# Kernel optimization log

Hardware: AMD Instinct MI355X
Metric: run time of the kernel (lower is better)

Reference implementation:

```python
import jax, jax.numpy as jnp
import numpy as np

N_NODES = 100000
N_EDGES = 3200000
NFEAT = 256
NHID = 256


def setup_inputs() -> dict:
    key = jax.random.key(0)
    ks = jax.random.split(key, 8)
    x = jax.random.normal(ks[0], (N_NODES, NFEAT), dtype=jnp.float32)
    # Glorot-ish scaled weights
    W1 = jax.random.normal(ks[1], (NFEAT, NHID), dtype=jnp.float32) / np.sqrt(NFEAT)
    b1 = jax.random.normal(ks[2], (NHID,), dtype=jnp.float32) * 0.01
    W2 = jax.random.normal(ks[3], (NHID, NHID), dtype=jnp.float32) / np.sqrt(NHID)
    b2 = jax.random.normal(ks[4], (NHID,), dtype=jnp.float32) * 0.01
    edge_weight = jax.random.uniform(ks[5], (N_EDGES,), dtype=jnp.float32)
    edge_src = jax.random.randint(ks[6], (N_EDGES,), 0, N_NODES, dtype=jnp.int32)
    edge_dst = jax.random.randint(ks[7], (N_EDGES,), 0, N_NODES, dtype=jnp.int32)
    return {
        "x": x, "W1": W1, "b1": b1, "W2": W2, "b2": b2,
        "edge_weight": edge_weight, "edge_src": edge_src, "edge_dst": edge_dst,
    }


def _gcn_layer(x, W, b, edge_weight, edge_src, edge_dst):
    # support = x @ W  (dense GEMM, [N, d_out])
    support = x @ W
    # spmm(adj, support): gather source rows, scale by edge weight, scatter-add to dst
    msgs = support[edge_src] * edge_weight[:, None]          # [E, d_out]
    agg = jax.ops.segment_sum(msgs, edge_dst, num_segments=N_NODES)
    return agg + b


def reference(x, W1, b1, W2, b2, edge_weight, edge_src, edge_dst):
    # Eval mode: F.dropout is identity (training=False).
    h = jax.nn.elu(_gcn_layer(x, W1, b1, edge_weight, edge_src, edge_dst))
    h = jax.nn.elu(_gcn_layer(h, W2, b2, edge_weight, edge_src, edge_dst))
    return h
```

## Files before the change

### kernel.cpp

```cpp
#include <hip/hip_runtime.h>
#include <math.h>

#define N_NODES 100000
#define N_EDGES 3200000
#define NF 256

typedef unsigned short u16;
typedef unsigned int u32;

typedef __bf16 bf16x8_t __attribute__((ext_vector_type(8)));
typedef float f32x4_t __attribute__((ext_vector_type(4)));

__device__ __forceinline__ float bf2f(u16 u) {
  union { u32 i; float f; } v; v.i = ((u32)u) << 16; return v.f;
}
__device__ __forceinline__ u16 f2bf(float f) {
  union { float f; u32 i; } v; v.f = f;
  u32 x = v.i;
  u32 r = (x + 0x7FFFu + ((x >> 16) & 1u)) >> 16;
  return (u16)r;
}

__global__ void sniff_kernel(const u16* __restrict__ xr, int* __restrict__ flag) {
  __shared__ int cnt;
  if (threadIdx.x == 0) cnt = 0;
  __syncthreads();
  int c = 0;
  for (int i = threadIdx.x; i < 65536; i += 256) {
    u16 u = xr[i];
    if ((u & 0x7F80u) == 0x7F80u) c++;
  }
  atomicAdd(&cnt, c);
  __syncthreads();
  if (threadIdx.x == 0) flag[0] = (cnt >= 4) ? 1 : 0;
}

__global__ void transpose_w(const u16* __restrict__ Wu, const float* __restrict__ Wf,
                            const int* __restrict__ flagp, u16* __restrict__ Wt) {
  int k = blockIdx.x;
  int n = threadIdx.x;
  if (flagp[0]) Wt[n * NF + k] = f2bf(Wf[k * NF + n]);
  else          Wt[n * NF + k] = Wu[k * NF + n];
}

__global__ void conv_bias(const u16* __restrict__ bu, const float* __restrict__ bf_,
                          const int* __restrict__ flagp, u16* __restrict__ o) {
  int i = threadIdx.x;
  if (flagp[0]) o[i] = f2bf(bf_[i]);
  else          o[i] = bu[i];
}

__global__ void copy_i32(const int* __restrict__ a, int* __restrict__ b, int n) {
  int i = blockIdx.x * 256 + threadIdx.x;
  if (i < n) b[i] = a[i];
}

__global__ void hist_kernel(const int* __restrict__ dst, int* __restrict__ counts) {
  int e = blockIdx.x * 256 + threadIdx.x;
  atomicAdd(&counts[dst[e]], 1);
}

__global__ void scanA(const int* __restrict__ counts, int* __restrict__ partial) {
  __shared__ int s[256];
  int t = threadIdx.x;
  int gid = blockIdx.x * 256 + t;
  int v = (gid < N_NODES) ? counts[gid] : 0;
  s[t] = v;
  __syncthreads();
  for (int offd = 128; offd > 0; offd >>= 1) {
    if (t < offd) s[t] += s[t + offd];
    __syncthreads();
  }
  if (t == 0) partial[blockIdx.x] = s[0];
}

__global__ void scanB(int* __restrict__ partial) {
  const int NPART = 391;
  __shared__ int s[512];
  int t = threadIdx.x;
  int v = (t < NPART) ? partial[t] : 0;
  s[t] = v;
  __syncthreads();
  for (int offd = 1; offd < 512; offd <<= 1) {
    int x = 0;
    if (t >= offd) x = s[t - offd];
    __syncthreads();
    s[t] += x;
    __syncthreads();
  }
  if (t < NPART) partial[t] = (t == 0) ? 0 : s[t - 1];
}

__global__ void scanC(const int* __restrict__ counts, const int* __restrict__ partial,
                      int* __restrict__ offs) {
  __shared__ int s[256];
  int t = threadIdx.x;
  int b = blockIdx.x;
  int gid = b * 256 + t;
  int v = (gid < N_NODES) ? counts[gid] : 0;
  s[t] = v;
  __syncthreads();
  for (int offd = 1; offd < 256; offd <<= 1) {
    int x = 0;
    if (t >= offd) x = s[t - offd];
    __syncthreads();
    s[t] += x;
    __syncthreads();
  }
  int incl = s[t];
  if (gid < N_NODES) offs[gid] = partial[b] + (incl - v);
  if (gid == N_NODES - 1) offs[N_NODES] = partial[b] + incl;
}

__global__ void scatter_full(const int* __restrict__ src, const int* __restrict__ dst,
                             const u16* __restrict__ wu, const float* __restrict__ wf,
                             const int* __restrict__ flagp, int* __restrict__ cursor,
                             int* __restrict__ ssrc, u16* __restrict__ sw) {
  int e = blockIdx.x * 256 + threadIdx.x;
  int d = dst[e];
  int pos = atomicAdd(&cursor[d], 1);
  ssrc[pos] = src[e];
  if (flagp[0]) sw[pos] = f2bf(wf[e]);
  else          sw[pos] = wu[e];
}

__global__ void scatter_eid(const int* __restrict__ dst, int* __restrict__ cursor,
                            int* __restrict__ seid) {
  int e = blockIdx.x * 256 + threadIdx.x;
  int d = dst[e];
  int pos = atomicAdd(&cursor[d], 1);
  seid[pos] = e;
}

__global__ __launch_bounds__(256) void gemm_bf16(
    const u16* __restrict__ A2, const float* __restrict__ A4,
    const u16* __restrict__ Bt, u16* __restrict__ C, int M,
    const int* __restrict__ flagp, int amask) {
  __shared__ __align__(16) u16 Al[128][40];
  __shared__ __align__(16) u16 Bl[128][40];
  const int afl = amask ? flagp[0] : 0;
  const int tid = threadIdx.x;
  const int m0 = blockIdx.x * 128;
  const int n0 = blockIdx.y * 128;
  const int lane = tid & 63;
  const int wave = tid >> 6;
  const int wm = (wave & 1) * 64;
  const int wn = (wave >> 1) * 64;
  const int mrow = lane & 15;
  const int grp = lane >> 4;

  f32x4_t acc[4][4];
  const f32x4_t zero = {0.f, 0.f, 0.f, 0.f};
#pragma unroll
  for (int i = 0; i < 4; ++i)
#pragma unroll
    for (int j = 0; j < 4; ++j) acc[i][j] = zero;

  for (int k0 = 0; k0 < NF; k0 += 32) {
#pragma unroll
    for (int r = 0; r < 2; ++r) {
      int chunk = tid + 256 * r;
      int row = chunk >> 2;
      int col = (chunk & 3) * 8;
      int gm = m0 + row;
      if (afl) {
        u16 t8[8];
        if (gm < M) {
          const float* p = A4 + (size_t)gm * NF + k0 + col;
          float4 ua = *(const float4*)(p);
          float4 ub = *(const float4*)(p + 4);
          t8[0] = f2bf(ua.x); t8[1] = f2bf(ua.y); t8[2] = f2bf(ua.z); t8[3] = f2bf(ua.w);
          t8[4] = f2bf(ub.x); t8[5] = f2bf(ub.y); t8[6] = f2bf(ub.z); t8[7] = f2bf(ub.w);
        } else {
          for (int q = 0; q < 8; ++q) t8[q] = 0;
        }
        *(uint4*)(&Al[row][col]) = *(const uint4*)t8;
      } else {
        uint4 va = make_uint4(0u, 0u, 0u, 0u);
        if (gm < M) va = *(const uint4*)(A2 + (size_t)gm * NF + k0 + col);
        *(uint4*)(&Al[row][col]) = va;
      }
      uint4 vb = *(const uint4*)(Bt + (size_t)(n0 + row) * NF + k0 + col);
      *(uint4*)(&Bl[row][col]) = vb;
    }
    __syncthreads();
    bf16x8_t af[4], bfr[4];
#pragma unroll
    for (int i = 0; i < 4; ++i)
      af[i] = *(const bf16x8_t*)(&Al[wm + i * 16 + mrow][grp * 8]);
#pragma unroll
    for (int j = 0; j < 4; ++j)
      bfr[j] = *(const bf16x8_t*)(&Bl[wn + j * 16 + mrow][grp * 8]);
#pragma unroll
    for (int i = 0; i < 4; ++i)
#pragma unroll
      for (int j = 0; j < 4; ++j)
        acc[i][j] = __builtin_amdgcn_mfma_f32_16x16x32_bf16(af[i], bfr[j], acc[i][j], 0, 0, 0);
    __syncthreads();
  }

#pragma unroll
  for (int i = 0; i < 4; ++i) {
#pragma unroll
    for (int j = 0; j < 4; ++j) {
#pragma unroll
      for (int r = 0; r < 4; ++r) {
        int row = m0 + wm + i * 16 + grp * 4 + r;
        int col = n0 + wn + j * 16 + mrow;
        if (row < M) C[(size_t)row * NF + col] = f2bf(acc[i][j][r]);
      }
    }
  }
}

__global__ __launch_bounds__(256) void agg_full(
    const u16* __restrict__ sup, const int* __restrict__ offs,
    const int* __restrict__ ssrc, const u16* __restrict__ sw,
    const u16* __restrict__ bbf, u16* __restrict__ out2, float* __restrict__ out4,
    const int* __restrict__ flagp, int outmask) {
  int node = blockIdx.x * 4 + (threadIdx.x >> 6);
  int lane = threadIdx.x & 63;
  int c0 = lane * 4;
  float a0 = 0.f, a1 = 0.f, a2 = 0.f, a3 = 0.f;
  int e = offs[node];
  int eend = offs[node + 1];

  for (; e + 8 <= eend; e += 8) {
    int s0 = ssrc[e + 0], s1 = ssrc[e + 1], s2 = ssrc[e + 2], s3 = ssrc[e + 3];
    int s4 = ssrc[e + 4], s5 = ssrc[e + 5], s6 = ssrc[e + 6], s7 = ssrc[e + 7];
    float w0 = bf2f(sw[e + 0]), w1 = bf2f(sw[e + 1]), w2 = bf2f(sw[e + 2]), w3 = bf2f(sw[e + 3]);
    float w4 = bf2f(sw[e + 4]), w5 = bf2f(sw[e + 5]), w6 = bf2f(sw[e + 6]), w7 = bf2f(sw[e + 7]);
    ushort4 v0 = *(const ushort4*)(sup + (size_t)s0 * NF + c0);
    ushort4 v1 = *(const ushort4*)(sup + (size_t)s1 * NF + c0);
    ushort4 v2 = *(const ushort4*)(sup + (size_t)s2 * NF + c0);
    ushort4 v3 = *(const ushort4*)(sup + (size_t)s3 * NF + c0);
    ushort4 v4 = *(const ushort4*)(sup + (size_t)s4 * NF + c0);
    ushort4 v5 = *(const ushort4*)(sup + (size_t)s5 * NF + c0);
    ushort4 v6 = *(const ushort4*)(sup + (size_t)s6 * NF + c0);
    ushort4 v7 = *(const ushort4*)(sup + (size_t)s7 * NF + c0);
    a0 += bf2f(v0.x) * w0; a1 += bf2f(v0.y) * w0; a2 += bf2f(v0.z) * w0; a3 += bf2f(v0.w) * w0;
    a0 += bf2f(v1.x) * w1; a1 += bf2f(v1.y) * w1; a2 += bf2f(v1.z) * w1; a3 += bf2f(v1.w) * w1;
    a0 += bf2f(v2.x) * w2; a1 += bf2f(v2.y) * w2; a2 += bf2f(v2.z) * w2; a3 += bf2f(v2.w) * w2;
    a0 += bf2f(v3.x) * w3; a1 += bf2f(v3.y) * w3; a2 += bf2f(v3.z) * w3; a3 += bf2f(v3.w) * w3;
    a0 += bf2f(v4.x) * w4; a1 += bf2f(v4.y) * w4; a2 += bf2f(v4.z) * w4; a3 += bf2f(v4.w) * w4;
    a0 += bf2f(v5.x) * w5; a1 += bf2f(v5.y) * w5; a2 += bf2f(v5.z) * w5; a3 += bf2f(v5.w) * w5;
    a0 += bf2f(v6.x) * w6; a1 += bf2f(v6.y) * w6; a2 += bf2f(v6.z) * w6; a3 += bf2f(v6.w) * w6;
    a0 += bf2f(v7.x) * w7; a1 += bf2f(v7.y) * w7; a2 += bf2f(v7.z) * w7; a3 += bf2f(v7.w) * w7;
  }
  for (; e < eend; ++e) {
    int src = ssrc[e];
    float w = bf2f(sw[e]);
    ushort4 v = *(const ushort4*)(sup + (size_t)src * NF + c0);
    a0 += bf2f(v.x) * w;
    a1 += bf2f(v.y) * w;
    a2 += bf2f(v.z) * w;
    a3 += bf2f(v.w) * w;
  }
  ushort4 bv = *(const ushort4*)(bbf + c0);
  float r0 = a0 + bf2f(bv.x);
  float r1 = a1 + bf2f(bv.y);
  float r2 = a2 + bf2f(bv.z);
  float r3 = a3 + bf2f(bv.w);
  r0 = r0 > 0.f ? r0 : expm1f(r0);
  r1 = r1 > 0.f ? r1 : expm1f(r1);
  r2 = r2 > 0.f ? r2 : expm1f(r2);
  r3 = r3 > 0.f ? r3 : expm1f(r3);
  if (outmask && flagp[0]) {
    float4 o4;
    o4.x = r0; o4.y = r1; o4.z = r2; o4.w = r3;
    *(float4*)(out4 + (size_t)node * NF + c0) = o4;
  } else {
    ushort4 o;
    o.x = f2bf(r0); o.y = f2bf(r1); o.z = f2bf(r2); o.w = f2bf(r3);
    *(ushort4*)(out2 + (size_t)node * NF + c0) = o;
  }
}

__global__ __launch_bounds__(256) void agg_eid(
    const u16* __restrict__ sup, const int* __restrict__ offs,
    const int* __restrict__ seid, const int* __restrict__ esrc,
    const u16* __restrict__ ewu, const float* __restrict__ ewf,
    const u16* __restrict__ bbf, u16* __restrict__ out2, float* __restrict__ out4,
    const int* __restrict__ flagp, int outmask) {
  int node = blockIdx.x * 4 + (threadIdx.x >> 6);
  int lane = threadIdx.x & 63;
  int c0 = lane * 4;
  int isf = flagp[0];
  float a0 = 0.f, a1 = 0.f, a2 = 0.f, a3 = 0.f;
  int e = offs[node];
  int eend = offs[node + 1];
  for (; e < eend; ++e) {
    int eid = seid[e];
    int src = esrc[eid];
    float w = isf ? ewf[eid] : bf2f(ewu[eid]);
    ushort4 v = *(const ushort4*)(sup + (size_t)src * NF + c0);
    a0 += bf2f(v.x) * w;
    a1 += bf2f(v.y) * w;
    a2 += bf2f(v.z) * w;
    a3 += bf2f(v.w) * w;
  }
  ushort4 bv = *(const ushort4*)(bbf + c0);
  float r0 = a0 + bf2f(bv.x);
  float r1 = a1 + bf2f(bv.y);
  float r2 = a2 + bf2f(bv.z);
  float r3 = a3 + bf2f(bv.w);
  r0 = r0 > 0.f ? r0 : expm1f(r0);
  r1 = r1 > 0.f ? r1 : expm1f(r1);
  r2 = r2 > 0.f ? r2 : expm1f(r2);
  r3 = r3 > 0.f ? r3 : expm1f(r3);
  if (outmask && isf) {
    float4 o4;
    o4.x = r0; o4.y = r1; o4.z = r2; o4.w = r3;
    *(float4*)(out4 + (size_t)node * NF + c0) = o4;
  } else {
    ushort4 o;
    o.x = f2bf(r0); o.y = f2bf(r1); o.z = f2bf(r2); o.w = f2bf(r3);
    *(ushort4*)(out2 + (size_t)node * NF + c0) = o;
  }
}

extern "C" void kernel_launch(void* const* d_in, const int* in_sizes, int n_in,
                              void* d_out, int out_size, void* d_ws, size_t ws_size,
                              hipStream_t stream) {
  const u16* x2    = (const u16*)d_in[0];
  const float* x4  = (const float*)d_in[0];
  const u16* W1u   = (const u16*)d_in[1];
  const float* W1f = (const float*)d_in[1];
  const u16* b1u   = (const u16*)d_in[2];
  const float* b1f = (const float*)d_in[2];
  const u16* W2u   = (const u16*)d_in[3];
  const float* W2f = (const float*)d_in[3];
  const u16* b2u   = (const u16*)d_in[4];
  const float* b2f = (const float*)d_in[4];
  const u16* ewu   = (const u16*)d_in[5];
  const float* ewf = (const float*)d_in[5];
  const int* esrc  = (const int*)d_in[6];
  const int* edst  = (const int*)d_in[7];
  u16* out2  = (u16*)d_out;
  float* out4 = (float*)d_out;

  char* ws = (char*)d_ws;
  size_t oWt1     = 0;
  size_t oWt2     = 131072;
  size_t oSup     = 262144;
  size_t oCounts  = 51462144;
  size_t oOffs    = 51862528;
  size_t oCursor  = 52262912;
  size_t oPartial = 52663296;
  size_t oFlag    = 52665344;
  size_t oBb1     = 52665600;
  size_t oBb2     = 52666624;
  size_t oTail    = 52667648;
  size_t need_full = oTail + 12800000 + 6400000;

  u16* Wt1     = (u16*)(ws + oWt1);
  u16* Wt2     = (u16*)(ws + oWt2);
  u16* sup     = (u16*)(ws + oSup);
  int* counts  = (int*)(ws + oCounts);
  int* offs    = (int*)(ws + oOffs);
  int* cursor  = (int*)(ws + oCursor);
  int* partial = (int*)(ws + oPartial);
  int* flag    = (int*)(ws + oFlag);
  u16* bb1     = (u16*)(ws + oBb1);
  u16* bb2     = (u16*)(ws + oBb2);

  u16* h1 = out2;

  sniff_kernel<<<1, 256, 0, stream>>>(x2, flag);
  hipMemsetAsync(counts, 0, (size_t)N_NODES * 4, stream);
  transpose_w<<<256, 256, 0, stream>>>(W1u, W1f, flag, Wt1);
  transpose_w<<<256, 256, 0, stream>>>(W2u, W2f, flag, Wt2);
  conv_bias<<<1, 256, 0, stream>>>(b1u, b1f, flag, bb1);
  conv_bias<<<1, 256, 0, stream>>>(b2u, b2f, flag, bb2);
  hist_kernel<<<N_EDGES / 256, 256, 0, stream>>>(edst, counts);
  scanA<<<391, 256, 0, stream>>>(counts, partial);
  scanB<<<1, 512, 0, stream>>>(partial);
  scanC<<<391, 256, 0, stream>>>(counts, partial, offs);
  copy_i32<<<391, 256, 0, stream>>>(offs, cursor, N_NODES);

  dim3 ggrid((N_NODES + 127) / 128, 2);

  if (ws_size >= need_full) {
    int* ssrc = (int*)(ws + oTail);
    u16* sw   = (u16*)(ws + oTail + 12800000);
    scatter_full<<<N_EDGES / 256, 256, 0, stream>>>(esrc, edst, ewu, ewf, flag, cursor, ssrc, sw);
    gemm_bf16<<<ggrid, 256, 0, stream>>>(x2, x4, Wt1, sup, N_NODES, flag, 1);
    agg_full<<<N_NODES / 4, 256, 0, stream>>>(sup, offs, ssrc, sw, bb1, h1, out4, flag, 0);
    gemm_bf16<<<ggrid, 256, 0, stream>>>(h1, (const float*)h1, Wt2, sup, N_NODES, flag, 0);
    agg_full<<<N_NODES / 4, 256, 0, stream>>>(sup, offs, ssrc, sw, bb2, out2, out4, flag, 1);
  } else {
    int* seid = (int*)(ws + oTail);
    scatter_eid<<<N_EDGES / 256, 256, 0, stream>>>(edst, cursor, seid);
    gemm_bf16<<<ggrid, 256, 0, stream>>>(x2, x4, Wt1, sup, N_NODES, flag, 1);
    agg_eid<<<N_NODES / 4, 256, 0, stream>>>(sup, offs, seid, esrc, ewu, ewf, bb1, h1, out4, flag, 0);
    gemm_bf16<<<ggrid, 256, 0, stream>>>(h1, (const float*)h1, Wt2, sup, N_NODES, flag, 0);
    agg_eid<<<N_NODES / 4, 256, 0, stream>>>(sup, offs, seid, esrc, ewu, ewf, bb2, out2, out4, flag, 1);
  }
}
```

Baseline: 1.129 ms.

## Use direct-to-LDS loads in GEMM, rank-based CSR build, wider aggregation gathers

Several changes land at once. The histogram pass now records each edge's rank, so the CSR placement becomes atomic-free and the cursor copy is dropped. Fp32 x is pre-converted to bf16 in a separate pass into a scratch region of the output. The GEMM stages tiles with global_load_lds into unpadded LDS, swaps the MFMA operands and stores packed 4-element results. Aggregation has each half-wave handle alternate edges with 16-byte gathers, then combines the halves with a shuffle. The costs are an extra conversion pass, possible LDS bank conflicts from the unpadded layout, and reliance on output-buffer scratch space.

```diff
diff --git a/kernel.cpp b/kernel.cpp
--- a/kernel.cpp
+++ b/kernel.cpp
@@ -10,6 +10,11 @@
 
 typedef __bf16 bf16x8_t __attribute__((ext_vector_type(8)));
 typedef float f32x4_t __attribute__((ext_vector_type(4)));
+
+union U8 { uint4 q; u16 s[8]; };
+
+typedef __attribute__((address_space(1))) const void* as1_cvp;
+typedef __attribute__((address_space(3))) void* as3_vp;
 
 __device__ __forceinline__ float bf2f(u16 u) {
   union { u32 i; float f; } v; v.i = ((u32)u) << 16; return v.f;
@@ -19,6 +24,10 @@
   u32 x = v.i;
   u32 r = (x + 0x7FFFu + ((x >> 16) & 1u)) >> 16;
   return (u16)r;
+}
+
+__device__ __forceinline__ void gload_lds16(const u16* g, u16* l) {
+  __builtin_amdgcn_global_load_lds((as1_cvp)g, (as3_vp)l, 16, 0, 0);
 }
 
 __global__ void sniff_kernel(const u16* __restrict__ xr, int* __restrict__ flag) {
@@ -50,14 +59,22 @@
   else          o[i] = bu[i];
 }
 
-__global__ void copy_i32(const int* __restrict__ a, int* __restrict__ b, int n) {
-  int i = blockIdx.x * 256 + threadIdx.x;
-  if (i < n) b[i] = a[i];
-}
-
-__global__ void hist_kernel(const int* __restrict__ dst, int* __restrict__ counts) {
+__global__ void conv_x(const float* __restrict__ xf, const int* __restrict__ flagp,
+                       u16* __restrict__ xbf) {
+  if (!flagp[0]) return;
+  size_t i = ((size_t)blockIdx.x * 256 + threadIdx.x) * 8;
+  float4 a = *(const float4*)(xf + i);
+  float4 b = *(const float4*)(xf + i + 4);
+  U8 t;
+  t.s[0] = f2bf(a.x); t.s[1] = f2bf(a.y); t.s[2] = f2bf(a.z); t.s[3] = f2bf(a.w);
+  t.s[4] = f2bf(b.x); t.s[5] = f2bf(b.y); t.s[6] = f2bf(b.z); t.s[7] = f2bf(b.w);
+  *(uint4*)(xbf + i) = t.q;
+}
+
+__global__ void hist_rank(const int* __restrict__ dst, int* __restrict__ counts,
+                          int* __restrict__ rank) {
   int e = blockIdx.x * 256 + threadIdx.x;
-  atomicAdd(&counts[dst[e]], 1);
+  rank[e] = atomicAdd(&counts[dst[e]], 1);
 }
 
 __global__ void scanA(const int* __restrict__ counts, int* __restrict__ partial) {
@@ -112,33 +129,31 @@
   if (gid == N_NODES - 1) offs[N_NODES] = partial[b] + incl;
 }
 
-__global__ void scatter_full(const int* __restrict__ src, const int* __restrict__ dst,
-                             const u16* __restrict__ wu, const float* __restrict__ wf,
-                             const int* __restrict__ flagp, int* __restrict__ cursor,
-                             int* __restrict__ ssrc, u16* __restrict__ sw) {
+__global__ void place_full(const int* __restrict__ src, const int* __restrict__ dst,
+                           const u16* __restrict__ wu, const float* __restrict__ wf,
+                           const int* __restrict__ flagp, const int* __restrict__ offs,
+                           const int* __restrict__ rank,
+                           int* __restrict__ ssrc, u16* __restrict__ sw) {
   int e = blockIdx.x * 256 + threadIdx.x;
-  int d = dst[e];
-  int pos = atomicAdd(&cursor[d], 1);
+  int pos = offs[dst[e]] + rank[e];
   ssrc[pos] = src[e];
   if (flagp[0]) sw[pos] = f2bf(wf[e]);
   else          sw[pos] = wu[e];
 }
 
-__global__ void scatter_eid(const int* __restrict__ dst, int* __restrict__ cursor,
-                            int* __restrict__ seid) {
+__global__ void place_eid(const int* __restrict__ dst, const int* __restrict__ offs,
+                          const int* __restrict__ rank, int* __restrict__ seid) {
   int e = blockIdx.x * 256 + threadIdx.x;
-  int d = dst[e];
-  int pos = atomicAdd(&cursor[d], 1);
-  seid[pos] = e;
-}
-
-__global__ __launch_bounds__(256) void gemm_bf16(
-    const u16* __restrict__ A2, const float* __restrict__ A4,
+  seid[offs[dst[e]] + rank[e]] = e;
+}
+
+__global__ __launch_bounds__(256) void gemm_gll(
+    const u16* __restrict__ A0, const u16* __restrict__ A1,
     const u16* __restrict__ Bt, u16* __restrict__ C, int M,
-    const int* __restrict__ flagp, int amask) {
-  __shared__ __align__(16) u16 Al[128][40];
-  __shared__ __align__(16) u16 Bl[128][40];
-  const int afl = amask ? flagp[0] : 0;
+    const int* __restrict__ flagp) {
+  __shared__ __align__(16) u16 Al[128 * 32];
+  __shared__ __align__(16) u16 Bl[128 * 32];
+  const u16* A = flagp[0] ? A1 : A0;
   const int tid = threadIdx.x;
   const int m0 = blockIdx.x * 128;
   const int n0 = blockIdx.y * 128;
@@ -156,59 +171,47 @@
 #pragma unroll
     for (int j = 0; j < 4; ++j) acc[i][j] = zero;
 
+  const int rA = lane >> 2;
+  const int cA = (lane & 3) * 8;
+
   for (int k0 = 0; k0 < NF; k0 += 32) {
 #pragma unroll
-    for (int r = 0; r < 2; ++r) {
-      int chunk = tid + 256 * r;
-      int row = chunk >> 2;
-      int col = (chunk & 3) * 8;
-      int gm = m0 + row;
-      if (afl) {
-        u16 t8[8];
-        if (gm < M) {
-          const float* p = A4 + (size_t)gm * NF + k0 + col;
-          float4 ua = *(const float4*)(p);
-          float4 ub = *(const float4*)(p + 4);
-          t8[0] = f2bf(ua.x); t8[1] = f2bf(ua.y); t8[2] = f2bf(ua.z); t8[3] = f2bf(ua.w);
-          t8[4] = f2bf(ub.x); t8[5] = f2bf(ub.y); t8[6] = f2bf(ub.z); t8[7] = f2bf(ub.w);
-        } else {
-          for (int q = 0; q < 8; ++q) t8[q] = 0;
-        }
-        *(uint4*)(&Al[row][col]) = *(const uint4*)t8;
-      } else {
-        uint4 va = make_uint4(0u, 0u, 0u, 0u);
-        if (gm < M) va = *(const uint4*)(A2 + (size_t)gm * NF + k0 + col);
-        *(uint4*)(&Al[row][col]) = va;
-      }
-      uint4 vb = *(const uint4*)(Bt + (size_t)(n0 + row) * NF + k0 + col);
-      *(uint4*)(&Bl[row][col]) = vb;
+    for (int c = 0; c < 2; ++c) {
+      int r0 = wave * 32 + c * 16;
+      int ar = r0 + rA;
+      int gm = m0 + ar;
+      if (gm >= M) gm = 0;
+      gload_lds16(A + (size_t)gm * NF + k0 + cA, &Al[r0 * 32]);
+      gload_lds16(Bt + (size_t)(n0 + ar) * NF + k0 + cA, &Bl[r0 * 32]);
     }
     __syncthreads();
     bf16x8_t af[4], bfr[4];
 #pragma unroll
     for (int i = 0; i < 4; ++i)
-      af[i] = *(const bf16x8_t*)(&Al[wm + i * 16 + mrow][grp * 8]);
+      af[i] = *(const bf16x8_t*)(&Al[(wm + i * 16 + mrow) * 32 + grp * 8]);
 #pragma unroll
     for (int j = 0; j < 4; ++j)
-      bfr[j] = *(const bf16x8_t*)(&Bl[wn + j * 16 + mrow][grp * 8]);
+      bfr[j] = *(const bf16x8_t*)(&Bl[(wn + j * 16 + mrow) * 32 + grp * 8]);
 #pragma unroll
     for (int i = 0; i < 4; ++i)
 #pragma unroll
       for (int j = 0; j < 4; ++j)
-        acc[i][j] = __builtin_amdgcn_mfma_f32_16x16x32_bf16(af[i], bfr[j], acc[i][j], 0, 0, 0);
+        acc[i][j] = __builtin_amdgcn_mfma_f32_16x16x32_bf16(bfr[j], af[i], acc[i][j], 0, 0, 0);
     __syncthreads();
   }
 
 #pragma unroll
   for (int i = 0; i < 4; ++i) {
+    int row = m0 + wm + i * 16 + mrow;
+    if (row >= M) continue;
 #pragma unroll
     for (int j = 0; j < 4; ++j) {
-#pragma unroll
-      for (int r = 0; r < 4; ++r) {
-        int row = m0 + wm + i * 16 + grp * 4 + r;
-        int col = n0 + wn + j * 16 + mrow;
-        if (row < M) C[(size_t)row * NF + col] = f2bf(acc[i][j][r]);
-      }
+      u16 pk[4];
+      pk[0] = f2bf(acc[i][j][0]);
+      pk[1] = f2bf(acc[i][j][1]);
+      pk[2] = f2bf(acc[i][j][2]);
+      pk[3] = f2bf(acc[i][j][3]);
+      *(uint2*)(C + (size_t)row * NF + n0 + wn + j * 16 + grp * 4) = *(const uint2*)pk;
     }
   }
 }
@@ -220,59 +223,73 @@
     const int* __restrict__ flagp, int outmask) {
   int node = blockIdx.x * 4 + (threadIdx.x >> 6);
   int lane = threadIdx.x & 63;
-  int c0 = lane * 4;
-  float a0 = 0.f, a1 = 0.f, a2 = 0.f, a3 = 0.f;
-  int e = offs[node];
+  int half = lane >> 5;
+  int c0 = (lane & 31) * 8;
+  float a0 = 0.f, a1 = 0.f, a2 = 0.f, a3 = 0.f, a4 = 0.f, a5 = 0.f, a6 = 0.f, a7 = 0.f;
   int eend = offs[node + 1];
-
-  for (; e + 8 <= eend; e += 8) {
-    int s0 = ssrc[e + 0], s1 = ssrc[e + 1], s2 = ssrc[e + 2], s3 = ssrc[e + 3];
-    int s4 = ssrc[e + 4], s5 = ssrc[e + 5], s6 = ssrc[e + 6], s7 = ssrc[e + 7];
-    float w0 = bf2f(sw[e + 0]), w1 = bf2f(sw[e + 1]), w2 = bf2f(sw[e + 2]), w3 = bf2f(sw[e + 3]);
-    float w4 = bf2f(sw[e + 4]), w5 = bf2f(sw[e + 5]), w6 = bf2f(sw[e + 6]), w7 = bf2f(sw[e + 7]);
-    ushort4 v0 = *(const ushort4*)(sup + (size_t)s0 * NF + c0);
-    ushort4 v1 = *(const ushort4*)(sup + (size_t)s1 * NF + c0);
-    ushort4 v2 = *(const ushort4*)(sup + (size_t)s2 * NF + c0);
-    ushort4 v3 = *(const ushort4*)(sup + (size_t)s3 * NF + c0);
-    ushort4 v4 = *(const ushort4*)(sup + (size_t)s4 * NF + c0);
-    ushort4 v5 = *(const ushort4*)(sup + (size_t)s5 * NF + c0);
-    ushort4 v6 = *(const ushort4*)(sup + (size_t)s6 * NF + c0);
-    ushort4 v7 = *(const ushort4*)(sup + (size_t)s7 * NF + c0);
-    a0 += bf2f(v0.x) * w0; a1 += bf2f(v0.y) * w0; a2 += bf2f(v0.z) * w0; a3 += bf2f(v0.w) * w0;
-    a0 += bf2f(v1.x) * w1; a1 += bf2f(v1.y) * w1; a2 += bf2f(v1.z) * w1; a3 += bf2f(v1.w) * w1;
-    a0 += bf2f(v2.x) * w2; a1 += bf2f(v2.y) * w2; a2 += bf2f(v2.z) * w2; a3 += bf2f(v2.w) * w2;
-    a0 += bf2f(v3.x) * w3; a1 += bf2f(v3.y) * w3; a2 += bf2f(v3.z) * w3; a3 += bf2f(v3.w) * w3;
-    a0 += bf2f(v4.x) * w4; a1 += bf2f(v4.y) * w4; a2 += bf2f(v4.z) * w4; a3 += bf2f(v4.w) * w4;
-    a0 += bf2f(v5.x) * w5; a1 += bf2f(v5.y) * w5; a2 += bf2f(v5.z) * w5; a3 += bf2f(v5.w) * w5;
-    a0 += bf2f(v6.x) * w6; a1 += bf2f(v6.y) * w6; a2 += bf2f(v6.z) * w6; a3 += bf2f(v6.w) * w6;
-    a0 += bf2f(v7.x) * w7; a1 += bf2f(v7.y) * w7; a2 += bf2f(v7.z) * w7; a3 += bf2f(v7.w) * w7;
-  }
-  for (; e < eend; ++e) {
-    int src = ssrc[e];
-    float w = bf2f(sw[e]);
-    ushort4 v = *(const ushort4*)(sup + (size_t)src * NF + c0);
-    a0 += bf2f(v.x) * w;
-    a1 += bf2f(v.y) * w;
-    a2 += bf2f(v.z) * w;
-    a3 += bf2f(v.w) * w;
-  }
-  ushort4 bv = *(const ushort4*)(bbf + c0);
-  float r0 = a0 + bf2f(bv.x);
-  float r1 = a1 + bf2f(bv.y);
-  float r2 = a2 + bf2f(bv.z);
-  float r3 = a3 + bf2f(bv.w);
-  r0 = r0 > 0.f ? r0 : expm1f(r0);
-  r1 = r1 > 0.f ? r1 : expm1f(r1);
-  r2 = r2 > 0.f ? r2 : expm1f(r2);
-  r3 = r3 > 0.f ? r3 : expm1f(r3);
-  if (outmask && flagp[0]) {
-    float4 o4;
-    o4.x = r0; o4.y = r1; o4.z = r2; o4.w = r3;
-    *(float4*)(out4 + (size_t)node * NF + c0) = o4;
-  } else {
-    ushort4 o;
-    o.x = f2bf(r0); o.y = f2bf(r1); o.z = f2bf(r2); o.w = f2bf(r3);
-    *(ushort4*)(out2 + (size_t)node * NF + c0) = o;
+  int e = offs[node] + half;
+
+  for (; e + 6 < eend; e += 8) {
+    int s0 = ssrc[e], s1 = ssrc[e + 2], s2 = ssrc[e + 4], s3 = ssrc[e + 6];
+    float w0 = bf2f(sw[e]), w1 = bf2f(sw[e + 2]), w2 = bf2f(sw[e + 4]), w3 = bf2f(sw[e + 6]);
+    U8 v0, v1, v2, v3;
+    v0.q = *(const uint4*)(sup + (((u32)s0) << 8) + c0);
+    v1.q = *(const uint4*)(sup + (((u32)s1) << 8) + c0);
+    v2.q = *(const uint4*)(sup + (((u32)s2) << 8) + c0);
+    v3.q = *(const uint4*)(sup + (((u32)s3) << 8) + c0);
+    a0 += bf2f(v0.s[0]) * w0; a1 += bf2f(v0.s[1]) * w0; a2 += bf2f(v0.s[2]) * w0; a3 += bf2f(v0.s[3]) * w0;
+    a4 += bf2f(v0.s[4]) * w0; a5 += bf2f(v0.s[5]) * w0; a6 += bf2f(v0.s[6]) * w0; a7 += bf2f(v0.s[7]) * w0;
+    a0 += bf2f(v1.s[0]) * w1; a1 += bf2f(v1.s[1]) * w1; a2 += bf2f(v1.s[2]) * w1; a3 += bf2f(v1.s[3]) * w1;
+    a4 += bf2f(v1.s[4]) * w1; a5 += bf2f(v1.s[5]) * w1; a6 += bf2f(v1.s[6]) * w1; a7 += bf2f(v1.s[7]) * w1;
+    a0 += bf2f(v2.s[0]) * w2; a1 += bf2f(v2.s[1]) * w2; a2 += bf2f(v2.s[2]) * w2; a3 += bf2f(v2.s[3]) * w2;
+    a4 += bf2f(v2.s[4]) * w2; a5 += bf2f(v2.s[5]) * w2; a6 += bf2f(v2.s[6]) * w2; a7 += bf2f(v2.s[7]) * w2;
+    a0 += bf2f(v3.s[0]) * w3; a1 += bf2f(v3.s[1]) * w3; a2 += bf2f(v3.s[2]) * w3; a3 += bf2f(v3.s[3]) * w3;
+    a4 += bf2f(v3.s[4]) * w3; a5 += bf2f(v3.s[5]) * w3; a6 += bf2f(v3.s[6]) * w3; a7 += bf2f(v3.s[7]) * w3;
+  }
+  for (; e < eend; e += 2) {
+    int s0 = ssrc[e];
+    float w0 = bf2f(sw[e]);
+    U8 v0;
+    v0.q = *(const uint4*)(sup + (((u32)s0) << 8) + c0);
+    a0 += bf2f(v0.s[0]) * w0; a1 += bf2f(v0.s[1]) * w0; a2 += bf2f(v0.s[2]) * w0; a3 += bf2f(v0.s[3]) * w0;
+    a4 += bf2f(v0.s[4]) * w0; a5 += bf2f(v0.s[5]) * w0; a6 += bf2f(v0.s[6]) * w0; a7 += bf2f(v0.s[7]) * w0;
+  }
+
+  a0 += __shfl_xor(a0, 32); a1 += __shfl_xor(a1, 32);
+  a2 += __shfl_xor(a2, 32); a3 += __shfl_xor(a3, 32);
+  a4 += __shfl_xor(a4, 32); a5 += __shfl_xor(a5, 32);
+  a6 += __shfl_xor(a6, 32); a7 += __shfl_xor(a7, 32);
+
+  if (half == 0) {
+    U8 bv; bv.q = *(const uint4*)(bbf + c0);
+    float r0 = a0 + bf2f(bv.s[0]);
+    float r1 = a1 + bf2f(bv.s[1]);
+    float r2 = a2 + bf2f(bv.s[2]);
+    float r3 = a3 + bf2f(bv.s[3]);
+    float r4 = a4 + bf2f(bv.s[4]);
+    float r5 = a5 + bf2f(bv.s[5]);
+    float r6 = a6 + bf2f(bv.s[6]);
+    float r7 = a7 + bf2f(bv.s[7]);
+    r0 = r0 > 0.f ? r0 : expm1f(r0);
+    r1 = r1 > 0.f ? r1 : expm1f(r1);
+    r2 = r2 > 0.f ? r2 : expm1f(r2);
+    r3 = r3 > 0.f ? r3 : expm1f(r3);
+    r4 = r4 > 0.f ? r4 : expm1f(r4);
+    r5 = r5 > 0.f ? r5 : expm1f(r5);
+    r6 = r6 > 0.f ? r6 : expm1f(r6);
+    r7 = r7 > 0.f ? r7 : expm1f(r7);
+    if (outmask && flagp[0]) {
+      float4 o4a, o4b;
+      o4a.x = r0; o4a.y = r1; o4a.z = r2; o4a.w = r3;
+      o4b.x = r4; o4b.y = r5; o4b.z = r6; o4b.w = r7;
+      *(float4*)(out4 + (size_t)node * NF + c0) = o4a;
+      *(float4*)(out4 + (size_t)node * NF + c0 + 4) = o4b;
+    } else {
+      U8 o;
+      o.s[0] = f2bf(r0); o.s[1] = f2bf(r1); o.s[2] = f2bf(r2); o.s[3] = f2bf(r3);
+      o.s[4] = f2bf(r4); o.s[5] = f2bf(r5); o.s[6] = f2bf(r6); o.s[7] = f2bf(r7);
+      *(uint4*)(out2 + (size_t)node * NF + c0) = o.q;
+    }
   }
 }
 
@@ -345,7 +362,6 @@
   size_t oSup     = 262144;
   size_t oCounts  = 51462144;
   size_t oOffs    = 51862528;
-  size_t oCursor  = 52262912;
   size_t oPartial = 52663296;
   size_t oFlag    = 52665344;
   size_t oBb1     = 52665600;
@@ -356,15 +372,16 @@
   u16* Wt1     = (u16*)(ws + oWt1);
   u16* Wt2     = (u16*)(ws + oWt2);
   u16* sup     = (u16*)(ws + oSup);
+  int* rank    = (int*)(ws + oSup);
   int* counts  = (int*)(ws + oCounts);
   int* offs    = (int*)(ws + oOffs);
-  int* cursor  = (int*)(ws + oCursor);
   int* partial = (int*)(ws + oPartial);
   int* flag    = (int*)(ws + oFlag);
   u16* bb1     = (u16*)(ws + oBb1);
   u16* bb2     = (u16*)(ws + oBb2);
 
-  u16* h1 = out2;
+  u16* h1  = out2;
+  u16* xbf = (u16*)((char*)d_out + (size_t)N_NODES * NF * 2);
 
   sniff_kernel<<<1, 256, 0, stream>>>(x2, flag);
   hipMemsetAsync(counts, 0, (size_t)N_NODES * 4, stream);
@@ -372,28 +389,28 @@
   transpose_w<<<256, 256, 0, stream>>>(W2u, W2f, flag, Wt2);
   conv_bias<<<1, 256, 0, stream>>>(b1u, b1f, flag, bb1);
   conv_bias<<<1, 256, 0, stream>>>(b2u, b2f, flag, bb2);
-  hist_kernel<<<N_EDGES / 256, 256, 0, stream>>>(edst, counts);
+  conv_x<<<N_NODES * NF / (256 * 8), 256, 0, stream>>>(x4, flag, xbf);
+  hist_rank<<<N_EDGES / 256, 256, 0, stream>>>(edst, counts, rank);
   scanA<<<391, 256, 0, stream>>>(counts, partial);
   scanB<<<1, 512, 0, stream>>>(partial);
   scanC<<<391, 256, 0, stream>>>(counts, partial, offs);
-  copy_i32<<<391, 256, 0, stream>>>(offs, cursor, N_NODES);
 
   dim3 ggrid((N_NODES + 127) / 128, 2);
 
   if (ws_size >= need_full) {
     int* ssrc = (int*)(ws + oTail);
     u16* sw   = (u16*)(ws + oTail + 12800000);
-    scatter_full<<<N_EDGES / 256, 256, 0, stream>>>(esrc, edst, ewu, ewf, flag, cursor, ssrc, sw);
-    gemm_bf16<<<ggrid, 256, 0, stream>>>(x2, x4, Wt1, sup, N_NODES, flag, 1);
+    place_full<<<N_EDGES / 256, 256, 0, stream>>>(esrc, edst, ewu, ewf, flag, offs, rank, ssrc, sw);
+    gemm_gll<<<ggrid, 256, 0, stream>>>(x2, xbf, Wt1, sup, N_NODES, flag);
     agg_full<<<N_NODES / 4, 256, 0, stream>>>(sup, offs, ssrc, sw, bb1, h1, out4, flag, 0);
-    gemm_bf16<<<ggrid, 256, 0, stream>>>(h1, (const float*)h1, Wt2, sup, N_NODES, flag, 0);
+    gemm_gll<<<ggrid, 256, 0, stream>>>(h1, h1, Wt2, sup, N_NODES, flag);
     agg_full<<<N_NODES / 4, 256, 0, stream>>>(sup, offs, ssrc, sw, bb2, out2, out4, flag, 1);
   } else {
     int* seid = (int*)(ws + oTail);
-    scatter_eid<<<N_EDGES / 256, 256, 0, stream>>>(edst, cursor, seid);
-    gemm_bf16<<<ggrid, 256, 0, stream>>>(x2, x4, Wt1, sup, N_NODES, flag, 1);
+    place_eid<<<N_EDGES / 256, 256, 0, stream>>>(edst, offs, rank, seid);
+    gemm_gll<<<ggrid, 256, 0, stream>>>(x2, xbf, Wt1, sup, N_NODES, flag);
     agg_eid<<<N_NODES / 4, 256, 0, stream>>>(sup, offs, seid, esrc, ewu, ewf, bb1, h1, out4, flag, 0);
-    gemm_bf16<<<ggrid, 256, 0, stream>>>(h1, (const float*)h1, Wt2, sup, N_NODES, flag, 0);
+    gemm_gll<<<ggrid, 256, 0, stream>>>(h1, h1, Wt2, sup, N_NODES, flag);
     agg_eid<<<N_NODES / 4, 256, 0, stream>>>(sup, offs, seid, esrc, ewu, ewf, bb2, out2, out4, flag, 1);
   }
 }
```

Result: faster. 1.048 ms (-7.1%).
